# Kernel tuning notes

Measured on AMD Instinct MI355X. Metric: run time of the kernel, lower is better.

The kernel has to match this reference:

```python
import jax, jax.numpy as jnp
import numpy as np

D_MODEL = 1024
RANK = 256
INIT_ALPHA = 0.5


def setup_inputs() -> dict:
    key = jax.random.key(0)
    ks = jax.random.split(key, 12)
    D, R = D_MODEL, RANK
    s = 0.02
    return {
        "x": jax.random.normal(ks[0], (4, 2048, D), dtype=jnp.float32),
        "Wq": jax.random.normal(ks[1], (D, D), dtype=jnp.float32) * s,
        "Wk": jax.random.normal(ks[2], (D, D), dtype=jnp.float32) * s,
        "Wo": jax.random.normal(ks[3], (D, D), dtype=jnp.float32) * s,
        "U_b": jax.random.normal(ks[4], (D, R), dtype=jnp.float32) * s,
        "V_b": jax.random.normal(ks[5], (D, R), dtype=jnp.float32) * s,
        "W_b": jax.random.normal(ks[6], (D, R), dtype=jnp.float32) * s,
        "bias_b": jnp.zeros((D,), dtype=jnp.float32),
        "U_t": jax.random.normal(ks[7], (D, R), dtype=jnp.float32) * s,
        "V_t": jax.random.normal(ks[8], (D, R), dtype=jnp.float32) * s,
        "W_t": jax.random.normal(ks[9], (D, R), dtype=jnp.float32) * s,
        "X_t": jax.random.normal(ks[10], (D, R), dtype=jnp.float32) * s,
        "bias_t": jnp.zeros((D,), dtype=jnp.float32),
        "alpha": jnp.asarray(INIT_ALPHA, dtype=jnp.float32),
    }


def reference(x, Wq, Wk, Wo, U_b, V_b, W_b, bias_b, U_t, V_t, W_t, X_t, bias_t, alpha):
    # Math identical to the original O(T^2 D) materialization (attention_mask=None path),
    # reduced to causal cumulative sums: sum_{j<=i} (q_i * k_j) = q_i * cumsum_j(k_j).
    B, T, D = x.shape
    Q = x @ Wq.T                      # [B,T,D] (nn.Linear: x @ W^T)
    K = x @ Wk.T
    counts = jnp.arange(1, T + 1, dtype=x.dtype)[None, :, None]  # [1,T,1]
    Z = jnp.cumsum(x, axis=1) / counts  # causal cumulative mean [B,T,D]

    # Bilinear: sum_{j<=i} ((Q_i V_b) * (K_j W_b)) U_b^T + bias_b (per j)
    a_b = Q @ V_b                     # [B,T,R]
    c_b = jnp.cumsum(K @ W_b, axis=1) # [B,T,R] causal sum over j
    bil = (a_b * c_b) @ U_b.T         # [B,T,D]

    # Trilinear: sum_{j<=i} ((Q_i V_t) * (K_j W_t) * (Z_i X_t)) U_t^T + bias_t
    a_t = Q @ V_t
    c_t = jnp.cumsum(K @ W_t, axis=1)
    z_t = Z @ X_t
    tri = (a_t * z_t * c_t) @ U_t.T   # [B,T,D]

    # Per-i division by n_valid = i+1; the per-(i,j) biases average back to themselves.
    out = (bil + alpha * tri) / counts + (bias_b + alpha * bias_t)
    return out @ Wo.T                 # W_O (dropout=0 -> identity)
```

## Files before the change

### kernel.cpp

```cpp
#include <hip/hip_runtime.h>

#define NBATCH  4
#define TSEQ    2048
#define MROWS   8192
#define NCAT    1280
#define NE      512

#define OFF_WQT   0u
#define OFF_WKT   524288u
#define OFF_WOB   1048576u
#define OFF_VCT   1572864u
#define OFF_WCT   1835008u
#define OFF_UCT   2097152u
#define OFF_B2    2359296u
#define OFF_PB    2360320u
#define OFF_GB    3015680u
#define OFF_Y     3277824u
#define OFF_SCR   13763584u
#define OFF_XB    13861888u
#define OFF_EB    OFF_XB

typedef __attribute__((ext_vector_type(8))) short bf16x8;
typedef __attribute__((ext_vector_type(4))) float f32x4;

__device__ __forceinline__ unsigned short f2bf(float f) {
  union { float f; unsigned u; } v; v.f = f;
  return (unsigned short)((v.u + 0x7fff + ((v.u >> 16) & 1)) >> 16);
}
__device__ __forceinline__ float bf2f(unsigned short u) {
  union { unsigned u; float f; } v; v.u = ((unsigned)u) << 16;
  return v.f;
}

__device__ __forceinline__ void gload16(const void* g, void* l) {
  __builtin_amdgcn_global_load_lds(
      (const __attribute__((address_space(1))) unsigned*)g,
      (__attribute__((address_space(3))) unsigned*)l, 16, 0, 0);
}

template <int EPI, int OBF, int CS>
__device__ __forceinline__ void mfma_tile(
    const short* __restrict__ A, const short* __restrict__ B, void* __restrict__ Cv,
    int K, int ldA, int ldB, int ldC, int m0, int n0,
    const float* __restrict__ bias, float* __restrict__ scr, short* L) {
  const int tid = threadIdx.x;
  const int l = tid & 63;
  const int wv = tid >> 6;
  const int wm = (wv >> 1) * 64, wn = (wv & 1) * 64;
  const int srow = tid >> 3;
  const int schk = tid & 7;
  const int arow = wm + (l & 15), brow = wn + (l & 15);
  const int kq = l >> 4;

  f32x4 acc[4][4] = {};

#define STAGE(k0, buf) do {                                                  \
    short* As_ = L + (buf) * 16384;                                          \
    short* Bs_ = As_ + 8192;                                                 \
    _Pragma("unroll")                                                        \
    for (int p = 0; p < 4; ++p) {                                            \
      const int r = p * 32 + srow;                                           \
      const int sw = (schk ^ (r & 7)) * 8;                                   \
      gload16(A + (size_t)(m0 + r) * ldA + (k0) + sw, As_ + r * 64 + schk * 8); \
      gload16(B + (size_t)(n0 + r) * ldB + (k0) + sw, Bs_ + r * 64 + schk * 8); \
    }                                                                        \
  } while (0)

#define COMPUTE(buf) do {                                                    \
    short* As_ = L + (buf) * 16384;                                          \
    short* Bs_ = As_ + 8192;                                                 \
    _Pragma("unroll")                                                        \
    for (int h = 0; h < 2; ++h) {                                            \
      bf16x8 af[4], bfr[4];                                                  \
      _Pragma("unroll")                                                      \
      for (int m = 0; m < 4; ++m) {                                          \
        const int r = arow + m * 16;                                         \
        af[m] = *(const bf16x8*)&As_[r * 64 + (((h * 4 + kq) ^ (r & 7)) * 8)]; \
      }                                                                      \
      _Pragma("unroll")                                                      \
      for (int n = 0; n < 4; ++n) {                                          \
        const int r = brow + n * 16;                                         \
        bfr[n] = *(const bf16x8*)&Bs_[r * 64 + (((h * 4 + kq) ^ (r & 7)) * 8)]; \
      }                                                                      \
      _Pragma("unroll")                                                      \
      for (int m = 0; m < 4; ++m)                                            \
        _Pragma("unroll")                                                    \
        for (int n = 0; n < 4; ++n)                                          \
          acc[m][n] = __builtin_amdgcn_mfma_f32_16x16x32_bf16(af[m], bfr[n], acc[m][n], 0, 0, 0); \
    }                                                                        \
  } while (0)

  STAGE(0, 0);
  const int nt = K >> 6;
  for (int t = 0; t < nt; ++t) {
    if (t + 1 < nt) {
      STAGE((t + 1) << 6, (t + 1) & 1);
      asm volatile("s_waitcnt vmcnt(8)" ::: "memory");
    } else {
      asm volatile("s_waitcnt vmcnt(0)" ::: "memory");
    }
    asm volatile("s_barrier" ::: "memory");
    COMPUTE(t & 1);
    asm volatile("s_barrier" ::: "memory");
  }
#undef STAGE
#undef COMPUTE

  const int cc = wn + (l & 15);
  const int crb = wm + (l >> 4) * 4;
#pragma unroll
  for (int m = 0; m < 4; ++m) {
#pragma unroll
    for (int j = 0; j < 4; ++j) {
      const int gm = m0 + crb + m * 16 + j;
      float inv = 1.0f;
      if (EPI) inv = 1.0f / (float)((gm & (TSEQ - 1)) + 1);
#pragma unroll
      for (int n = 0; n < 4; ++n) {
        const int gn = n0 + cc + n * 16;
        float v = acc[m][n][j];
        if (EPI) v = v * inv + bias[gn];
        if (OBF) ((short*)Cv)[(size_t)gm * ldC + gn] = (short)f2bf(v);
        else     ((float*)Cv)[(size_t)gm * ldC + gn] = v;
      }
    }
  }
  if (CS && n0 >= 512) {
    const int bb = (m0 + wm) >> 11;
    const int seg = ((m0 + wm) & (TSEQ - 1)) >> 6;
    float* sp = scr + (size_t)(bb * 32 + seg) * 768 + (n0 - 512);
#pragma unroll
    for (int n = 0; n < 4; ++n) {
      float s = 0.f;
#pragma unroll
      for (int m = 0; m < 4; ++m)
#pragma unroll
        for (int j = 0; j < 4; ++j) s += acc[m][n][j];
      s += __shfl_xor(s, 16, 64);
      s += __shfl_xor(s, 32, 64);
      if (l < 16) sp[cc + n * 16] = s;
    }
  }
}

__device__ __forceinline__ void xcd_swizzle(int& bx, int& by) {
  const int gx = gridDim.x;
  const int nwg = gx * gridDim.y;
  const int n = by * gx + bx;
  const int q = nwg >> 3;
  const int s = (n & 7) * q + (n >> 3);
  bx = s % gx; by = s / gx;
}

template <int EPI, int OBF, int CS>
__global__ __launch_bounds__(256) void mfma_nt(
    const short* __restrict__ A, const short* __restrict__ B,
    void* __restrict__ C, int K, int ldA, int ldB, int ldC,
    const float* __restrict__ bias, float* __restrict__ scr) {
  __shared__ short L[32768];
  int bx = blockIdx.x, by = blockIdx.y;
  xcd_swizzle(bx, by);
  mfma_tile<EPI, OBF, CS>(A, B, C, K, ldA, ldB, ldC,
                          by * 128, bx * 128, bias, scr, L);
}

__global__ __launch_bounds__(256) void prep2(
    const short* __restrict__ VCT, const short* __restrict__ WQT,
    const short* __restrict__ WCT, const short* __restrict__ WKT,
    const short* __restrict__ WOB, const short* __restrict__ UCT,
    short* __restrict__ Pb, short* __restrict__ Gb,
    const float* __restrict__ x, short* __restrict__ xb) {
  __shared__ short L[32768];
  const int bid = blockIdx.x;
  if (bid >= 96) {
    const size_t j = ((size_t)(bid - 96) * 256 + threadIdx.x) * 4;
    const float4 v = *(const float4*)&x[j];
    ushort4 o;
    o.x = f2bf(v.x); o.y = f2bf(v.y); o.z = f2bf(v.z); o.w = f2bf(v.w);
    *(ushort4*)&((unsigned short*)xb)[j] = o;
    return;
  }
  const int g = bid >> 5, t = bid & 31;
  if (g == 0)
    mfma_tile<0, 1, 0>(VCT, WQT, Pb, 1024, 1024, 1024, 1024,
                       (t >> 3) * 128, (t & 7) * 128, nullptr, nullptr, L);
  else if (g == 1)
    mfma_tile<0, 1, 0>(WCT, WKT, Pb + (size_t)512 * 1024, 1024, 1024, 1024, 1024,
                       (t >> 3) * 128, (t & 7) * 128, nullptr, nullptr, L);
  else
    mfma_tile<0, 1, 0>(WOB, UCT, Gb, 1024, 1024, 1024, 512,
                       (t >> 2) * 128, (t & 3) * 128, nullptr, nullptr, L);
}

__global__ __launch_bounds__(256) void prep_all(
    const float* __restrict__ Vb, const float* __restrict__ Vt,
    const float* __restrict__ Wb, const float* __restrict__ Wt,
    const float* __restrict__ Ub, const float* __restrict__ Ut,
    const float* __restrict__ Xt, const float* __restrict__ Wq,
    const float* __restrict__ Wk, const float* __restrict__ Wo,
    const float* __restrict__ bias_b, const float* __restrict__ bias_t,
    const float* __restrict__ alpha_p,
    short* __restrict__ VCT, short* __restrict__ WCT, short* __restrict__ UCT,
    short* __restrict__ PbXt, short* __restrict__ WQT, short* __restrict__ WKT,
    short* __restrict__ WOB, float* __restrict__ b2) {
  const int bid = blockIdx.x;
  const int tid = threadIdx.x;
  if (bid >= 1984) {
    const float al = *alpha_p;
    const int d = bid - 1984;
    float s = 0.f;
    for (int e = tid; e < 1024; e += 256)
      s += Wo[(size_t)d * 1024 + e] * (bias_b[e] + al * bias_t[e]);
    __shared__ float red[256];
    red[tid] = s; __syncthreads();
    for (int off = 128; off > 0; off >>= 1) {
      if (tid < off) red[tid] += red[tid + off];
      __syncthreads();
    }
    if (tid == 0) b2[d] = red[0];
    return;
  }
  if (bid >= 960) {
    const size_t j = ((size_t)(bid - 960) * 256 + tid) * 4;
    const float4 v = *(const float4*)&Wo[j];
    ushort4 o;
    o.x = f2bf(v.x); o.y = f2bf(v.y); o.z = f2bf(v.z); o.w = f2bf(v.w);
    *(ushort4*)&((unsigned short*)WOB)[j] = o;
    return;
  }
  const float* src; short* O; int r0, d0, c0, ldS;
  if (bid < 384) {
    const int z = bid >> 7, t = bid & 127;
    r0 = (t >> 4) * 64; d0 = (t & 15) * 64; ldS = 256;
    const float* S0 = z == 0 ? Vb : z == 1 ? Wb : Ub;
    const float* S1 = z == 0 ? Vt : z == 1 ? Wt : Ut;
    O = z == 0 ? VCT : z == 1 ? WCT : UCT;
    src = (r0 < 256) ? S0 : S1; c0 = r0 & 255;
  } else if (bid < 448) {
    const int t = bid - 384;
    r0 = (t >> 4) * 64; d0 = (t & 15) * 64; ldS = 256;
    src = Xt; c0 = r0; O = PbXt;
  } else {
    const int t = bid - 448;
    const int w = t >> 8, tt = t & 255;
    r0 = (tt >> 4) * 64; d0 = (tt & 15) * 64; ldS = 1024;
    src = w ? Wk : Wq; O = w ? WKT : WQT; c0 = r0;
  }
  __shared__ float Ts[64][65];
  const int lr = tid >> 4;
  const int lc = (tid & 15) * 4;
#pragma unroll
  for (int p = 0; p < 4; ++p) {
    const int row = lr + p * 16;
    const float4 v = *(const float4*)&src[(size_t)(d0 + row) * ldS + c0 + lc];
    Ts[row][lc + 0] = v.x; Ts[row][lc + 1] = v.y;
    Ts[row][lc + 2] = v.z; Ts[row][lc + 3] = v.w;
  }
  __syncthreads();
#pragma unroll
  for (int p = 0; p < 4; ++p) {
    const int ri = lr + p * 16;
    ushort4 o;
    o.x = f2bf(Ts[lc + 0][ri]); o.y = f2bf(Ts[lc + 1][ri]);
    o.z = f2bf(Ts[lc + 2][ri]); o.w = f2bf(Ts[lc + 3][ri]);
    *(ushort4*)&((unsigned short*)O)[(size_t)(r0 + ri) * 1024 + d0 + lc] = o;
  }
}

#define LOADR(s, t) {                                                   \
    const unsigned short* p_ = yb + (size_t)(t) * NCAT;                 \
    ab##s = bf2f(p_[c2]);        at##s = bf2f(p_[256 + c2]);            \
    cb##s = bf2f(p_[512 + c2]);  ct##s = bf2f(p_[768 + c2]);            \
    zt##s = bf2f(p_[1024 + c2]); }
#define STEPR(s, t) {                                                   \
    run_cb += cb##s; run_ct += ct##s; run_zt += zt##s;                  \
    const float inv_ = 1.0f / (float)(segbase + (t) + 1);               \
    unsigned short* er_ = Eb + (row0 + (t)) * 512;                      \
    er_[c2]       = f2bf(ab##s * run_cb);                               \
    er_[256 + c2] = f2bf(al * at##s * (run_zt * inv_) * run_ct); }
__global__ __launch_bounds__(256) void scan_combine(
    const unsigned short* __restrict__ Y, const float* __restrict__ scr,
    unsigned short* __restrict__ Eb, const float* __restrict__ alpha_p) {
  const float al = *alpha_p;
  const int c2 = threadIdx.x;
  const int seg = blockIdx.x, b = blockIdx.y;
  const int segbase = seg * 64;
  float run_cb = 0.f, run_ct = 0.f, run_zt = 0.f;
  for (int s = 0; s < seg; ++s) {
    const float* sr = scr + (size_t)(b * 32 + s) * 768;
    run_cb += sr[c2]; run_ct += sr[256 + c2]; run_zt += sr[512 + c2];
  }
  const size_t row0 = (size_t)(b * TSEQ + segbase);
  const unsigned short* yb = Y + row0 * NCAT;
  float ab0, at0, cb0, ct0, zt0, ab1, at1, cb1, ct1, zt1;
  float ab2, at2, cb2, ct2, zt2, ab3, at3, cb3, ct3, zt3;
  float ab4, at4, cb4, ct4, zt4, ab5, at5, cb5, ct5, zt5;
  float ab6, at6, cb6, ct6, zt6, ab7, at7, cb7, ct7, zt7;
  LOADR(0, 0) LOADR(1, 1) LOADR(2, 2) LOADR(3, 3)
  LOADR(4, 4) LOADR(5, 5) LOADR(6, 6) LOADR(7, 7)
  for (int t = 0; t < 64; t += 8) {
    STEPR(0, t + 0) if (t + 8 < 64)  LOADR(0, t + 8)
    STEPR(1, t + 1) if (t + 9 < 64)  LOADR(1, t + 9)
    STEPR(2, t + 2) if (t + 10 < 64) LOADR(2, t + 10)
    STEPR(3, t + 3) if (t + 11 < 64) LOADR(3, t + 11)
    STEPR(4, t + 4) if (t + 12 < 64) LOADR(4, t + 12)
    STEPR(5, t + 5) if (t + 13 < 64) LOADR(5, t + 13)
    STEPR(6, t + 6) if (t + 14 < 64) LOADR(6, t + 14)
    STEPR(7, t + 7) if (t + 15 < 64) LOADR(7, t + 15)
  }
}
#undef LOADR
#undef STEPR

extern "C" void kernel_launch(void* const* d_in, const int* in_sizes, int n_in,
                              void* d_out, int out_size, void* d_ws, size_t ws_size,
                              hipStream_t stream) {
  const float* x      = (const float*)d_in[0];
  const float* Wq     = (const float*)d_in[1];
  const float* Wk     = (const float*)d_in[2];
  const float* Wo     = (const float*)d_in[3];
  const float* Ub     = (const float*)d_in[4];
  const float* Vb     = (const float*)d_in[5];
  const float* Wb     = (const float*)d_in[6];
  const float* bias_b = (const float*)d_in[7];
  const float* Ut     = (const float*)d_in[8];
  const float* Vt     = (const float*)d_in[9];
  const float* Wt     = (const float*)d_in[10];
  const float* Xt     = (const float*)d_in[11];
  const float* bias_t = (const float*)d_in[12];
  const float* alpha  = (const float*)d_in[13];
  float* out = (float*)d_out;
  float* ws  = (float*)d_ws;

  short* WQT = (short*)(ws + OFF_WQT);
  short* WKT = (short*)(ws + OFF_WKT);
  short* WOB = (short*)(ws + OFF_WOB);
  short* VCT = (short*)(ws + OFF_VCT);
  short* WCT = (short*)(ws + OFF_WCT);
  short* UCT = (short*)(ws + OFF_UCT);
  float* b2  = ws + OFF_B2;
  short* Pb  = (short*)(ws + OFF_PB);
  short* Gb  = (short*)(ws + OFF_GB);
  unsigned short* Yb = (unsigned short*)(ws + OFF_Y);
  float* scr = ws + OFF_SCR;
  short* xb  = (short*)(ws + OFF_XB);
  short* Eb  = (short*)(ws + OFF_EB);

  prep_all<<<3008, 256, 0, stream>>>(Vb, Vt, Wb, Wt, Ub, Ut, Xt, Wq, Wk, Wo,
                                     bias_b, bias_t, alpha,
                                     VCT, WCT, UCT, Pb + (size_t)1024 * 1024,
                                     WQT, WKT, WOB, b2);
  prep2<<<8288, 256, 0, stream>>>(VCT, WQT, WCT, WKT, WOB, UCT, Pb, Gb, x, xb);
  mfma_nt<0, 1, 1><<<dim3(NCAT / 128, MROWS / 128), 256, 0, stream>>>(
      xb, Pb, Yb, 1024, 1024, 1024, NCAT, nullptr, scr);
  scan_combine<<<dim3(32, NBATCH), 256, 0, stream>>>(Yb, scr, (unsigned short*)Eb, alpha);
  mfma_nt<1, 0, 0><<<dim3(1024 / 128, MROWS / 128), 256, 0, stream>>>(
      Eb, Gb, out, 512, 512, 512, 1024, b2, nullptr);
}
```

Measured before the change: 196.7 us.

## Use 256x256 tiles with 512-thread blocks and phased staging for main GEMMs

Replaces the 128x128, 256-thread GEMM kernel used for the two large matmuls with a 256x256-tile, 8-wave kernel. Each k-step is split into four phases that load the next tile's quarters while computing on the current buffer, and s_setprio is raised during the MFMA bursts. The goal is more operand reuse per LDS load and better overlap of global loads with compute. The cost is 128 KB of LDS per block and fewer workgroups: 160 for the first GEMM and 128 for the second, on a GPU with 256 CUs, which can leave many CUs idle.

New measurement: 219.3 us. +11.5%, slower.

```diff
diff --git a/kernel.cpp b/kernel.cpp
--- a/kernel.cpp
+++ b/kernel.cpp
@@ -38,11 +38,156 @@
       (__attribute__((address_space(3))) unsigned*)l, 16, 0, 0);
 }
 
+__device__ __forceinline__ void xcd_swizzle(int& bx, int& by) {
+  const int gx = gridDim.x;
+  const int nwg = gx * gridDim.y;
+  const int n = by * gx + bx;
+  const int q = nwg >> 3;
+  const int s = (n & 7) * q + (n >> 3);
+  bx = s % gx; by = s / gx;
+}
+
 template <int EPI, int OBF, int CS>
+__global__ __launch_bounds__(512, 2) void mfma_nt256(
+    const short* __restrict__ A, const short* __restrict__ B,
+    void* __restrict__ Cv, int K, int ldA, int ldB, int ldC,
+    const float* __restrict__ bias, float* __restrict__ scr) {
+  __shared__ short L[65536];
+  int bx = blockIdx.x, by = blockIdx.y;
+  xcd_swizzle(bx, by);
+  const int m0 = by * 256, n0 = bx * 256;
+  const int tid = threadIdx.x;
+  const int l = tid & 63;
+  const int wm2 = (tid >> 6) >> 2;
+  const int wn4 = (tid >> 6) & 3;
+  const int s_r = tid >> 3;
+  const int s_c = tid & 7;
+  const int fr = l & 15;
+  const int kq = l >> 4;
+
+  f32x4 acc[2][2][4][2] = {};
+  const int nt = K >> 6;
+
+#define STAGE_HT(kt, ht, d) do {                                             \
+    const int mat_ = (ht) & 1;                                               \
+    const int hf_ = (ht) >> 1;                                               \
+    short* dst_ = L + (d) * 32768 + mat_ * 16384 + hf_ * 8192;               \
+    const short* gs_ = mat_ ? B : A;                                         \
+    const int gb_ = mat_ ? n0 : m0;                                          \
+    const int ld_ = mat_ ? ldB : ldA;                                        \
+    _Pragma("unroll")                                                        \
+    for (int j_ = 0; j_ < 2; ++j_) {                                         \
+      const int rl_ = j_ * 64 + s_r;                                         \
+      const int rg_ = hf_ * 128 + rl_;                                       \
+      const int sw_ = (s_c ^ (rg_ & 7)) * 8;                                 \
+      gload16(gs_ + (size_t)(gb_ + rg_) * ld_ + (kt) * 64 + sw_,             \
+              dst_ + rl_ * 64 + s_c * 8);                                    \
+    }                                                                        \
+  } while (0)
+
+#define PHASE(t, p, mh, nh, TAILW) do {                                      \
+    const int d_ = (t) & 1;                                                  \
+    const short* As_ = L + d_ * 32768;                                       \
+    const short* Bs_ = As_ + 16384;                                          \
+    bf16x8 af_[4][2], bv_[2][2];                                             \
+    _Pragma("unroll")                                                        \
+    for (int mf_ = 0; mf_ < 4; ++mf_) {                                      \
+      const int ra_ = (mh) * 128 + wm2 * 64 + mf_ * 16 + fr;                 \
+      _Pragma("unroll")                                                      \
+      for (int kk_ = 0; kk_ < 2; ++kk_) {                                    \
+        const int q_ = kk_ * 4 + kq;                                         \
+        af_[mf_][kk_] = *(const bf16x8*)&As_[ra_ * 64 + ((q_ ^ (ra_ & 7)) * 8)]; \
+      }                                                                      \
+    }                                                                        \
+    _Pragma("unroll")                                                        \
+    for (int nf_ = 0; nf_ < 2; ++nf_) {                                      \
+      const int rb_ = (nh) * 128 + wn4 * 32 + nf_ * 16 + fr;                 \
+      _Pragma("unroll")                                                      \
+      for (int kk_ = 0; kk_ < 2; ++kk_) {                                    \
+        const int q_ = kk_ * 4 + kq;                                         \
+        bv_[nf_][kk_] = *(const bf16x8*)&Bs_[rb_ * 64 + ((q_ ^ (rb_ & 7)) * 8)]; \
+      }                                                                      \
+    }                                                                        \
+    if ((t) + 1 < nt) {                                                      \
+      STAGE_HT((t) + 1, p, d_ ^ 1);                                          \
+      asm volatile("s_waitcnt vmcnt(4)" ::: "memory");                       \
+    } else {                                                                 \
+      TAILW;                                                                 \
+    }                                                                        \
+    __builtin_amdgcn_s_barrier();                                            \
+    __builtin_amdgcn_s_setprio(1);                                           \
+    _Pragma("unroll")                                                        \
+    for (int kk_ = 0; kk_ < 2; ++kk_)                                        \
+      _Pragma("unroll")                                                      \
+      for (int mf_ = 0; mf_ < 4; ++mf_)                                      \
+        _Pragma("unroll")                                                    \
+        for (int nf_ = 0; nf_ < 2; ++nf_)                                    \
+          acc[mh][nh][mf_][nf_] = __builtin_amdgcn_mfma_f32_16x16x32_bf16(   \
+              af_[mf_][kk_], bv_[nf_][kk_], acc[mh][nh][mf_][nf_], 0, 0, 0); \
+    __builtin_amdgcn_s_setprio(0);                                           \
+    __builtin_amdgcn_s_barrier();                                            \
+  } while (0)
+
+  STAGE_HT(0, 0, 0); STAGE_HT(0, 1, 0); STAGE_HT(0, 2, 0); STAGE_HT(0, 3, 0);
+  asm volatile("s_waitcnt vmcnt(4)" ::: "memory");
+  __builtin_amdgcn_s_barrier();
+
+  for (int t = 0; t < nt; ++t) {
+    PHASE(t, 0, 0, 0, asm volatile("s_waitcnt vmcnt(2)" ::: "memory"));
+    PHASE(t, 1, 1, 0, asm volatile("s_waitcnt vmcnt(0)" ::: "memory"));
+    PHASE(t, 2, 0, 1, (void)0);
+    PHASE(t, 3, 1, 1, (void)0);
+  }
+#undef STAGE_HT
+#undef PHASE
+
+#pragma unroll
+  for (int mh = 0; mh < 2; ++mh)
+#pragma unroll
+    for (int nh = 0; nh < 2; ++nh) {
+#pragma unroll
+      for (int mf = 0; mf < 4; ++mf)
+#pragma unroll
+        for (int j = 0; j < 4; ++j) {
+          const int gm = m0 + mh * 128 + wm2 * 64 + mf * 16 + (l >> 4) * 4 + j;
+          float inv = 1.0f;
+          if (EPI) inv = 1.0f / (float)((gm & (TSEQ - 1)) + 1);
+#pragma unroll
+          for (int nf = 0; nf < 2; ++nf) {
+            const int gn = n0 + nh * 128 + wn4 * 32 + nf * 16 + (l & 15);
+            float v = acc[mh][nh][mf][nf][j];
+            if (EPI) v = v * inv + bias[gn];
+            if (OBF) ((short*)Cv)[(size_t)gm * ldC + gn] = (short)f2bf(v);
+            else     ((float*)Cv)[(size_t)gm * ldC + gn] = v;
+          }
+        }
+      if (CS) {
+        const int rowband = m0 + mh * 128 + wm2 * 64;
+        const int bb = rowband >> 11;
+        const int seg = (rowband >> 6) & 31;
+#pragma unroll
+        for (int nf = 0; nf < 2; ++nf) {
+          const int gc0 = n0 + nh * 128 + wn4 * 32 + nf * 16;
+          if (gc0 >= 512) {
+            float s = 0.f;
+#pragma unroll
+            for (int mf = 0; mf < 4; ++mf)
+#pragma unroll
+              for (int j = 0; j < 4; ++j) s += acc[mh][nh][mf][nf][j];
+            s += __shfl_xor(s, 16, 64);
+            s += __shfl_xor(s, 32, 64);
+            if (l < 16)
+              scr[(size_t)(bb * 32 + seg) * 768 + (gc0 + l - 512)] = s;
+          }
+        }
+      }
+    }
+}
+
+template <int OBF>
 __device__ __forceinline__ void mfma_tile(
     const short* __restrict__ A, const short* __restrict__ B, void* __restrict__ Cv,
-    int K, int ldA, int ldB, int ldC, int m0, int n0,
-    const float* __restrict__ bias, float* __restrict__ scr, short* L) {
+    int K, int ldA, int ldB, int ldC, int m0, int n0, short* L) {
   const int tid = threadIdx.x;
   const int l = tid & 63;
   const int wv = tid >> 6;
@@ -113,55 +258,15 @@
 #pragma unroll
     for (int j = 0; j < 4; ++j) {
       const int gm = m0 + crb + m * 16 + j;
-      float inv = 1.0f;
-      if (EPI) inv = 1.0f / (float)((gm & (TSEQ - 1)) + 1);
 #pragma unroll
       for (int n = 0; n < 4; ++n) {
         const int gn = n0 + cc + n * 16;
         float v = acc[m][n][j];
-        if (EPI) v = v * inv + bias[gn];
         if (OBF) ((short*)Cv)[(size_t)gm * ldC + gn] = (short)f2bf(v);
         else     ((float*)Cv)[(size_t)gm * ldC + gn] = v;
       }
     }
   }
-  if (CS && n0 >= 512) {
-    const int bb = (m0 + wm) >> 11;
-    const int seg = ((m0 + wm) & (TSEQ - 1)) >> 6;
-    float* sp = scr + (size_t)(bb * 32 + seg) * 768 + (n0 - 512);
-#pragma unroll
-    for (int n = 0; n < 4; ++n) {
-      float s = 0.f;
-#pragma unroll
-      for (int m = 0; m < 4; ++m)
-#pragma unroll
-        for (int j = 0; j < 4; ++j) s += acc[m][n][j];
-      s += __shfl_xor(s, 16, 64);
-      s += __shfl_xor(s, 32, 64);
-      if (l < 16) sp[cc + n * 16] = s;
-    }
-  }
-}
-
-__device__ __forceinline__ void xcd_swizzle(int& bx, int& by) {
-  const int gx = gridDim.x;
-  const int nwg = gx * gridDim.y;
-  const int n = by * gx + bx;
-  const int q = nwg >> 3;
-  const int s = (n & 7) * q + (n >> 3);
-  bx = s % gx; by = s / gx;
-}
-
-template <int EPI, int OBF, int CS>
-__global__ __launch_bounds__(256) void mfma_nt(
-    const short* __restrict__ A, const short* __restrict__ B,
-    void* __restrict__ C, int K, int ldA, int ldB, int ldC,
-    const float* __restrict__ bias, float* __restrict__ scr) {
-  __shared__ short L[32768];
-  int bx = blockIdx.x, by = blockIdx.y;
-  xcd_swizzle(bx, by);
-  mfma_tile<EPI, OBF, CS>(A, B, C, K, ldA, ldB, ldC,
-                          by * 128, bx * 128, bias, scr, L);
 }
 
 __global__ __launch_bounds__(256) void prep2(
@@ -182,14 +287,14 @@
   }
   const int g = bid >> 5, t = bid & 31;
   if (g == 0)
-    mfma_tile<0, 1, 0>(VCT, WQT, Pb, 1024, 1024, 1024, 1024,
-                       (t >> 3) * 128, (t & 7) * 128, nullptr, nullptr, L);
+    mfma_tile<1>(VCT, WQT, Pb, 1024, 1024, 1024, 1024,
+                 (t >> 3) * 128, (t & 7) * 128, L);
   else if (g == 1)
-    mfma_tile<0, 1, 0>(WCT, WKT, Pb + (size_t)512 * 1024, 1024, 1024, 1024, 1024,
-                       (t >> 3) * 128, (t & 7) * 128, nullptr, nullptr, L);
+    mfma_tile<1>(WCT, WKT, Pb + (size_t)512 * 1024, 1024, 1024, 1024, 1024,
+                 (t >> 3) * 128, (t & 7) * 128, L);
   else
-    mfma_tile<0, 1, 0>(WOB, UCT, Gb, 1024, 1024, 1024, 512,
-                       (t >> 2) * 128, (t & 3) * 128, nullptr, nullptr, L);
+    mfma_tile<1>(WOB, UCT, Gb, 1024, 1024, 1024, 512,
+                 (t >> 2) * 128, (t & 3) * 128, L);
 }
 
 __global__ __launch_bounds__(256) void prep_all(
@@ -351,9 +456,9 @@
                                      VCT, WCT, UCT, Pb + (size_t)1024 * 1024,
                                      WQT, WKT, WOB, b2);
   prep2<<<8288, 256, 0, stream>>>(VCT, WQT, WCT, WKT, WOB, UCT, Pb, Gb, x, xb);
-  mfma_nt<0, 1, 1><<<dim3(NCAT / 128, MROWS / 128), 256, 0, stream>>>(
+  mfma_nt256<0, 1, 1><<<dim3(NCAT / 256, MROWS / 256), 512, 0, stream>>>(
       xb, Pb, Yb, 1024, 1024, 1024, NCAT, nullptr, scr);
   scan_combine<<<dim3(32, NBATCH), 256, 0, stream>>>(Yb, scr, (unsigned short*)Eb, alpha);
-  mfma_nt<1, 0, 0><<<dim3(1024 / 128, MROWS / 128), 256, 0, stream>>>(
+  mfma_nt256<1, 0, 0><<<dim3(1024 / 256, MROWS / 256), 512, 0, stream>>>(
       Eb, Gb, out, 512, 512, 512, 1024, b2, nullptr);
 }
```
